# Kernel optimization log

Hardware: AMD Instinct MI355X
Metric: run time of the kernel (lower is better)

## Reference

```python
import jax, jax.numpy as jnp
import numpy as np

HEAD_DIM = 64
SCALE = 1.0 / np.sqrt(HEAD_DIM).astype(np.float32)


def setup_inputs() -> dict:
    key = jax.random.key(0)
    kq, kk, kv = jax.random.split(key, 3)
    shape = (2, 16, 2048, HEAD_DIM)  # [batch, num_heads, seq_len, head_dim]
    q = jax.random.normal(kq, shape, dtype=jnp.float32)
    k = jax.random.normal(kk, shape, dtype=jnp.float32)
    v = jax.random.normal(kv, shape, dtype=jnp.float32)
    # causal mask: True above the diagonal means 'masked' (no attention)
    mask = jnp.triu(jnp.ones((2048, 2048), dtype=bool), k=1)
    return {"q": q, "k": k, "v": v, "mask": mask}


def reference(q, k, v, mask):
    # scores: [b, h, s, s]
    scores = jnp.einsum("bhqd,bhkd->bhqk", q, k) * SCALE
    scores = jnp.where(mask[None, None, :, :], -jnp.inf, scores)
    attn_weights = jax.nn.softmax(scores, axis=-1)
    attn_weights = jnp.where(mask[None, None, :, :], 0.0, attn_weights)
    output = jnp.einsum("bhqk,bhkd->bhqd", attn_weights, v)
    return (output, attn_weights)
```

## Files before the change

### kernel.cpp

```cpp
#include <hip/hip_runtime.h>
#include <stdint.h>


#define SEQ 2048
#define HD  64
#define NBH 32

typedef __attribute__((ext_vector_type(8))) short short8;
typedef __attribute__((ext_vector_type(4))) float f32x4;

static __device__ __forceinline__ short f2bf(float x) {
  uint32_t u = __builtin_bit_cast(uint32_t, x);
  u = (u + 0x7FFFu + ((u >> 16) & 1u)) >> 16;
  return (short)(uint16_t)u;
}
static __device__ __forceinline__ float bf2f(short h) {
  uint32_t u = ((uint32_t)(uint16_t)h) << 16;
  return __builtin_bit_cast(float, u);
}
static __device__ __forceinline__ int swz(int row, int col) {
  return (row << 6) + (col ^ ((row & 7) << 3));
}

#define MFMA16(a, b, c) __builtin_amdgcn_mfma_f32_16x16x32_bf16((a), (b), (c), 0, 0, 0)

#define GLOAD16(gsrc, ldst)                                             \
  __builtin_amdgcn_global_load_lds(                                     \
      (const __attribute__((address_space(1))) void*)(gsrc),            \
      (__attribute__((address_space(3))) void*)(ldst), 16, 0, 0)

static __device__ __forceinline__ void cvt4(const f32x4 x, short8& h, short8& l,
                                            const int base) {
#pragma unroll
  for (int j = 0; j < 4; ++j) {
    const float fv = x[j];
    const short hb = f2bf(fv);
    h[base + j] = hb;
    l[base + j] = f2bf(fv - bf2f(hb));
  }
}

__global__ void prep_k(const float* __restrict__ K, short* __restrict__ Kh,
                       short* __restrict__ Kl) {
  const int gidx = blockIdx.x * 256 + threadIdx.x;
  const int row = gidx >> 3, g = gidx & 7;
  const f32x4* s = (const f32x4*)(K + (size_t)row * HD + g * 8);
  short8 h, l;
  cvt4(s[0], h, l, 0);
  cvt4(s[1], h, l, 4);
  const size_t di = (size_t)row * HD + ((g ^ (row & 7)) << 3);
  *(short8*)&Kh[di] = h;
  *(short8*)&Kl[di] = l;
}

__global__ void prep_v(const float* __restrict__ V, short* __restrict__ Vh,
                       short* __restrict__ Vl) {
  __shared__ float t[64][65];
  const int bh = blockIdx.x >> 5, kt = blockIdx.x & 31;
  const float* src = V + ((size_t)bh * SEQ + kt * 64) * HD;
#pragma unroll
  for (int i = 0; i < 4; ++i) {
    const int ch = threadIdx.x + i * 256;
    const int r = ch >> 4, c4 = (ch & 15) << 2;
    const f32x4 x = *(const f32x4*)(src + r * HD + c4);
#pragma unroll
    for (int j = 0; j < 4; ++j) t[r][c4 + j] = x[j];
  }
  __syncthreads();
#pragma unroll
  for (int i = 0; i < 2; ++i) {
    const int oid = threadIdx.x + i * 256;
    const int d = oid >> 3, g = oid & 7;
    f32x4 a, b;
#pragma unroll
    for (int j = 0; j < 4; ++j) {
      a[j] = t[g * 8 + j][d];
      b[j] = t[g * 8 + 4 + j][d];
    }
    short8 h, l;
    cvt4(a, h, l, 0);
    cvt4(b, h, l, 4);
    const size_t di = ((size_t)bh * HD + d) * SEQ + kt * 64 + ((g ^ (d & 7)) << 3);
    *(short8*)&Vh[di] = h;
    *(short8*)&Vl[di] = l;
  }
}

__global__ __launch_bounds__(256, 2) void attn_fwd(
    const float* __restrict__ gq,
    const short* __restrict__ gKh, const short* __restrict__ gKl,
    const short* __restrict__ gVh, const short* __restrict__ gVl,
    float* __restrict__ go, float* __restrict__ ga) {
  __shared__ __align__(16) short lK[2][2][4096];
  __shared__ __align__(16) short lV[2][2][4096];
  __shared__ __align__(16) short lP[2][4][1024];

  const int tid  = threadIdx.x;
  const int w    = tid >> 6;
  const int lane = tid & 63;
  const int lg   = lane >> 4;
  const int ln   = lane & 15;

  const int bh = blockIdx.x >> 4;
  const int z  = blockIdx.x & 15;

  const float* qp  = gq  + (size_t)bh * SEQ * HD;
  const short* Khb = gKh + (size_t)bh * SEQ * HD;
  const short* Klb = gKl + (size_t)bh * SEQ * HD;
  const short* Vhb = gVh + (size_t)bh * SEQ * HD;
  const short* Vlb = gVl + (size_t)bh * SEQ * HD;
  float* op = go + (size_t)bh * SEQ * HD;
  float* ap = ga + (size_t)bh * SEQ * SEQ;

  auto stage_k = [&](const short* th, const short* tl, short* bh_, short* bl_) {
    const int o0 = w * 1024 + lane * 8;
    GLOAD16(th + o0,       bh_ + w * 1024);
    GLOAD16(th + o0 + 512, bh_ + w * 1024 + 512);
    GLOAD16(tl + o0,       bl_ + w * 1024);
    GLOAD16(tl + o0 + 512, bl_ + w * 1024 + 512);
  };
  auto stage_v = [&](const short* th, const short* tl, short* bh_, short* bl_) {
    const int c0 = w * 128 + lane;
    const int c1 = c0 + 64;
    GLOAD16(th + (size_t)(c0 >> 3) * SEQ + (c0 & 7) * 8, bh_ + w * 1024);
    GLOAD16(th + (size_t)(c1 >> 3) * SEQ + (c1 & 7) * 8, bh_ + w * 1024 + 512);
    GLOAD16(tl + (size_t)(c0 >> 3) * SEQ + (c0 & 7) * 8, bl_ + w * 1024);
    GLOAD16(tl + (size_t)(c1 >> 3) * SEQ + (c1 & 7) * 8, bl_ + w * 1024 + 512);
  };

  for (int sec = 0; sec < 2; ++sec) {
    const int qb     = (sec == 0) ? (31 - z) : z;
    const int qbase  = qb << 6;
    const int wqbase = qbase + (w << 4);

    short8 qh[2], ql[2];
    {
      const float* qrow = qp + (size_t)(wqbase + ln) * HD;
#pragma unroll
      for (int c = 0; c < 2; ++c) {
        const int d0 = c * 32 + lg * 8;
        const f32x4 x0 = *(const f32x4*)(qrow + d0);
        const f32x4 x1 = *(const f32x4*)(qrow + d0 + 4);
#pragma unroll
        for (int j = 0; j < 4; ++j) {
          float xs = x0[j] * 0.125f;
          short hb = f2bf(xs);
          qh[c][j] = hb;
          ql[c][j] = f2bf(xs - bf2f(hb));
          xs = x1[j] * 0.125f;
          hb = f2bf(xs);
          qh[c][4 + j] = hb;
          ql[c][4 + j] = f2bf(xs - bf2f(hb));
        }
      }
    }

    f32x4 oacc[4];
    const f32x4 Z4 = {0.f, 0.f, 0.f, 0.f};
#pragma unroll
    for (int n = 0; n < 4; ++n) oacc[n] = Z4;
    float lpart[4] = {0.f, 0.f, 0.f, 0.f};

    stage_k(Khb, Klb, lK[0][0], lK[0][1]);
    stage_v(Vhb, Vlb, lV[0][0], lV[0][1]);
    __syncthreads();
    int cur = 0;
    for (int kt = 0; kt <= qb; ++kt, cur ^= 1) {
      if (kt < qb) {
        stage_k(Khb + (kt + 1) * 4096, Klb + (kt + 1) * 4096,
                lK[cur ^ 1][0], lK[cur ^ 1][1]);
        stage_v(Vhb + (kt + 1) * 64, Vlb + (kt + 1) * 64,
                lV[cur ^ 1][0], lV[cur ^ 1][1]);
      }
      const short* bKh = lK[cur][0];
      const short* bKl = lK[cur][1];
      const short* bVh = lV[cur][0];
      const short* bVl = lV[cur][1];

      f32x4 sc[4];
#pragma unroll
      for (int n = 0; n < 4; ++n) {
        f32x4 acc = Z4;
#pragma unroll
        for (int c = 0; c < 2; ++c) {
          const int bi = swz(n * 16 + ln, c * 32 + lg * 8);
          const short8 kh = *(const short8*)&bKh[bi];
          const short8 kl = *(const short8*)&bKl[bi];
          acc = MFMA16(qh[c], kh, acc);
          acc = MFMA16(ql[c], kh, acc);
          acc = MFMA16(qh[c], kl, acc);
        }
        sc[n] = acc;
      }

#pragma unroll
      for (int n = 0; n < 4; ++n) {
        const int kg = (kt << 6) + n * 16 + ln;
#pragma unroll
        for (int r = 0; r < 4; ++r) {
          const int qg = wqbase + lg * 4 + r;
          const float e = (kg <= qg) ? __expf(sc[n][r]) : 0.f;
          lpart[r] += e;
          const short eh = f2bf(e);
          const short el = f2bf(e - bf2f(eh));
          const int pi = swz(lg * 4 + r, n * 16 + ln);
          lP[0][w][pi] = eh;
          lP[1][w][pi] = el;
        }
      }
      asm volatile("s_waitcnt lgkmcnt(0)" ::: "memory");
      __builtin_amdgcn_sched_barrier(0);

#pragma unroll
      for (int c = 0; c < 2; ++c) {
        const int ac = swz(ln, c * 32 + lg * 8);
        const short8 ph = *(const short8*)&lP[0][w][ac];
        const short8 pl = *(const short8*)&lP[1][w][ac];
#pragma unroll
        for (int n = 0; n < 4; ++n) {
          const int bi = swz(n * 16 + ln, c * 32 + lg * 8);
          const short8 vh = *(const short8*)&bVh[bi];
          const short8 vl = *(const short8*)&bVl[bi];
          oacc[n] = MFMA16(ph, vh, oacc[n]);
          oacc[n] = MFMA16(pl, vh, oacc[n]);
          oacc[n] = MFMA16(ph, vl, oacc[n]);
        }
      }
      __syncthreads();
    }

    float linv[4];
#pragma unroll
    for (int r = 0; r < 4; ++r) {
      float s = lpart[r];
      s += __shfl_xor(s, 8, 64);
      s += __shfl_xor(s, 4, 64);
      s += __shfl_xor(s, 2, 64);
      s += __shfl_xor(s, 1, 64);
      linv[r] = 1.0f / s;
    }

#pragma unroll
    for (int n = 0; n < 4; ++n)
#pragma unroll
      for (int r = 0; r < 4; ++r)
        __builtin_nontemporal_store(oacc[n][r] * linv[r],
            &op[(size_t)(wqbase + lg * 4 + r) * HD + n * 16 + ln]);

    stage_k(Khb, Klb, lK[0][0], lK[0][1]);
    __syncthreads();
    cur = 0;
    for (int kt = 0; kt <= qb; ++kt, cur ^= 1) {
      if (kt < qb)
        stage_k(Khb + (kt + 1) * 4096, Klb + (kt + 1) * 4096,
                lK[cur ^ 1][0], lK[cur ^ 1][1]);
      const short* bKh = lK[cur][0];
      const short* bKl = lK[cur][1];

      f32x4 sc[4];
#pragma unroll
      for (int n = 0; n < 4; ++n) {
        f32x4 acc = Z4;
#pragma unroll
        for (int c = 0; c < 2; ++c) {
          const int bi = swz(n * 16 + ln, c * 32 + lg * 8);
          const short8 kh = *(const short8*)&bKh[bi];
          const short8 kl = *(const short8*)&bKl[bi];
          acc = MFMA16(qh[c], kh, acc);
          acc = MFMA16(ql[c], kh, acc);
          acc = MFMA16(qh[c], kl, acc);
        }
        sc[n] = acc;
      }

#pragma unroll
      for (int n = 0; n < 4; ++n) {
        const int kg = (kt << 6) + n * 16 + ln;
#pragma unroll
        for (int r = 0; r < 4; ++r) {
          const int qg = wqbase + lg * 4 + r;
          const float pv = (kg <= qg) ? __expf(sc[n][r]) * linv[r] : 0.f;
          __builtin_nontemporal_store(pv, &ap[(size_t)qg * SEQ + kg]);
        }
      }
      __syncthreads();
    }

    const int zstart = (qb + 1) << 6;
    const int zc = SEQ - zstart;
    if (zc > 0) {
      for (int row = 0; row < 64; ++row) {
        float* dst = ap + (size_t)(qbase + row) * SEQ + zstart;
        for (int c = tid * 4; c < zc; c += 1024) {
          float* p = dst + c;
          __builtin_nontemporal_store(0.0f, p + 0);
          __builtin_nontemporal_store(0.0f, p + 1);
          __builtin_nontemporal_store(0.0f, p + 2);
          __builtin_nontemporal_store(0.0f, p + 3);
        }
      }
    }
  }
}

extern "C" void kernel_launch(void* const* d_in, const int* in_sizes, int n_in,
                              void* d_out, int out_size, void* d_ws, size_t ws_size,
                              hipStream_t stream) {
  (void)in_sizes; (void)n_in; (void)out_size; (void)ws_size;
  const float* q = (const float*)d_in[0];
  const float* k = (const float*)d_in[1];
  const float* v = (const float*)d_in[2];
  float* o = (float*)d_out;
  float* a = o + (size_t)NBH * SEQ * HD;

  short* Khi  = (short*)d_ws;
  short* Klo  = Khi  + (size_t)NBH * SEQ * HD;
  short* Vthi = Klo  + (size_t)NBH * SEQ * HD;
  short* Vtlo = Vthi + (size_t)NBH * SEQ * HD;

  prep_k<<<dim3(2048), dim3(256), 0, stream>>>(k, Khi, Klo);
  prep_v<<<dim3(1024), dim3(256), 0, stream>>>(v, Vthi, Vtlo);
  attn_fwd<<<dim3(512), dim3(256), 0, stream>>>(q, Khi, Klo, Vthi, Vtlo, o, a);
}
```

Before: 704.3 us.

## Restructure attention into 128-thread blocks with 32-key tiles and per-wave 32 query rows

Each block now has 2 waves handling one 64-row query tile, with each wave owning 32 query rows. Key tiles shrink to 32, and the grid grows to 1024 blocks, replacing the paired-section scheme with a direct mapping from block to query tile. The P tile is kept in LDS as fp32 and split into bf16 hi/lo on read, and the LDS swizzle moves from the prep kernels into the staging addresses. Zero-fill of the masked region uses vector stores. This is meant to raise MFMA reuse per loaded K/V fragment and improve occupancy and load balance, at the cost of more barriers per key and register pressure from doubled accumulators.

```diff
diff --git a/kernel.cpp b/kernel.cpp
--- a/kernel.cpp
+++ b/kernel.cpp
@@ -17,9 +17,6 @@
 static __device__ __forceinline__ float bf2f(short h) {
   uint32_t u = ((uint32_t)(uint16_t)h) << 16;
   return __builtin_bit_cast(float, u);
-}
-static __device__ __forceinline__ int swz(int row, int col) {
-  return (row << 6) + (col ^ ((row & 7) << 3));
 }
 
 #define MFMA16(a, b, c) __builtin_amdgcn_mfma_f32_16x16x32_bf16((a), (b), (c), 0, 0, 0)
@@ -48,7 +45,7 @@
   short8 h, l;
   cvt4(s[0], h, l, 0);
   cvt4(s[1], h, l, 4);
-  const size_t di = (size_t)row * HD + ((g ^ (row & 7)) << 3);
+  const size_t di = (size_t)row * HD + g * 8;
   *(short8*)&Kh[di] = h;
   *(short8*)&Kl[di] = l;
 }
@@ -80,20 +77,20 @@
     short8 h, l;
     cvt4(a, h, l, 0);
     cvt4(b, h, l, 4);
-    const size_t di = ((size_t)bh * HD + d) * SEQ + kt * 64 + ((g ^ (d & 7)) << 3);
+    const size_t di = ((size_t)bh * HD + d) * SEQ + kt * 64 + g * 8;
     *(short8*)&Vh[di] = h;
     *(short8*)&Vl[di] = l;
   }
 }
 
-__global__ __launch_bounds__(256, 2) void attn_fwd(
+__global__ __launch_bounds__(128, 2) void attn_fwd(
     const float* __restrict__ gq,
     const short* __restrict__ gKh, const short* __restrict__ gKl,
     const short* __restrict__ gVh, const short* __restrict__ gVl,
     float* __restrict__ go, float* __restrict__ ga) {
-  __shared__ __align__(16) short lK[2][2][4096];
-  __shared__ __align__(16) short lV[2][2][4096];
-  __shared__ __align__(16) short lP[2][4][1024];
+  __shared__ __align__(16) short lK[2][2][2048];
+  __shared__ __align__(16) short lVt[2][2][2048];
+  __shared__ __align__(16) float lP[2][1024];
 
   const int tid  = threadIdx.x;
   const int w    = tid >> 6;
@@ -101,8 +98,10 @@
   const int lg   = lane >> 4;
   const int ln   = lane & 15;
 
-  const int bh = blockIdx.x >> 4;
-  const int z  = blockIdx.x & 15;
+  const int i  = blockIdx.x >> 5;
+  const int bh = blockIdx.x & 31;
+  const int s  = (i < 16) ? (31 - i) : (i - 16);
+  const int nt = 2 * s + 2;
 
   const float* qp  = gq  + (size_t)bh * SEQ * HD;
   const short* Khb = gKh + (size_t)bh * SEQ * HD;
@@ -112,193 +111,215 @@
   float* op = go + (size_t)bh * SEQ * HD;
   float* ap = ga + (size_t)bh * SEQ * SEQ;
 
-  auto stage_k = [&](const short* th, const short* tl, short* bh_, short* bl_) {
-    const int o0 = w * 1024 + lane * 8;
-    GLOAD16(th + o0,       bh_ + w * 1024);
-    GLOAD16(th + o0 + 512, bh_ + w * 1024 + 512);
-    GLOAD16(tl + o0,       bl_ + w * 1024);
-    GLOAD16(tl + o0 + 512, bl_ + w * 1024 + 512);
+  const int wqb = s * 64 + w * 32;
+
+  short8 qh[2][2], ql[2][2];
+#pragma unroll
+  for (int gq2 = 0; gq2 < 2; ++gq2) {
+    const float* qrow = qp + (size_t)(wqb + gq2 * 16 + ln) * HD;
+#pragma unroll
+    for (int c = 0; c < 2; ++c) {
+      const int d0 = c * 32 + lg * 8;
+      const f32x4 x0 = *(const f32x4*)(qrow + d0);
+      const f32x4 x1 = *(const f32x4*)(qrow + d0 + 4);
+#pragma unroll
+      for (int j = 0; j < 4; ++j) {
+        float xs = x0[j] * 0.125f;
+        short hb = f2bf(xs);
+        qh[gq2][c][j] = hb;
+        ql[gq2][c][j] = f2bf(xs - bf2f(hb));
+        xs = x1[j] * 0.125f;
+        hb = f2bf(xs);
+        qh[gq2][c][4 + j] = hb;
+        ql[gq2][c][4 + j] = f2bf(xs - bf2f(hb));
+      }
+    }
+  }
+
+  auto stage_k = [&](int kt, int buf) {
+#pragma unroll
+    for (int j2 = 0; j2 < 2; ++j2) {
+      const int kr   = w * 16 + j2 * 8 + (lane >> 3);
+      const int sblk = (lane & 7) ^ (kr & 7);
+      const size_t so = (size_t)(kt * 32 + kr) * HD + sblk * 8;
+      GLOAD16(Khb + so, &lK[buf][0][w * 1024 + j2 * 512]);
+      GLOAD16(Klb + so, &lK[buf][1][w * 1024 + j2 * 512]);
+    }
   };
-  auto stage_v = [&](const short* th, const short* tl, short* bh_, short* bl_) {
-    const int c0 = w * 128 + lane;
-    const int c1 = c0 + 64;
-    GLOAD16(th + (size_t)(c0 >> 3) * SEQ + (c0 & 7) * 8, bh_ + w * 1024);
-    GLOAD16(th + (size_t)(c1 >> 3) * SEQ + (c1 & 7) * 8, bh_ + w * 1024 + 512);
-    GLOAD16(tl + (size_t)(c0 >> 3) * SEQ + (c0 & 7) * 8, bl_ + w * 1024);
-    GLOAD16(tl + (size_t)(c1 >> 3) * SEQ + (c1 & 7) * 8, bl_ + w * 1024 + 512);
+  auto stage_v = [&](int kt, int buf) {
+#pragma unroll
+    for (int j2 = 0; j2 < 2; ++j2) {
+      const int d   = j2 * 32 + w * 16 + (lane >> 2);
+      const int skb = (lane & 3) ^ ((d >> 1) & 3);
+      const size_t so = (size_t)d * SEQ + kt * 32 + skb * 8;
+      GLOAD16(Vhb + so, &lVt[buf][0][j2 * 1024 + w * 512]);
+      GLOAD16(Vlb + so, &lVt[buf][1][j2 * 1024 + w * 512]);
+    }
   };
 
-  for (int sec = 0; sec < 2; ++sec) {
-    const int qb     = (sec == 0) ? (31 - z) : z;
-    const int qbase  = qb << 6;
-    const int wqbase = qbase + (w << 4);
-
-    short8 qh[2], ql[2];
-    {
-      const float* qrow = qp + (size_t)(wqbase + ln) * HD;
+  f32x4 oacc[2][4];
+  const f32x4 Z4 = {0.f, 0.f, 0.f, 0.f};
+#pragma unroll
+  for (int a = 0; a < 2; ++a)
+#pragma unroll
+    for (int n = 0; n < 4; ++n) oacc[a][n] = Z4;
+  float lpart[2][4] = {{0.f, 0.f, 0.f, 0.f}, {0.f, 0.f, 0.f, 0.f}};
+
+  stage_k(0, 0);
+  stage_v(0, 0);
+  __syncthreads();
+  for (int kt = 0; kt < nt; ++kt) {
+    const int cur = kt & 1;
+    if (kt + 1 < nt) {
+      stage_k(kt + 1, cur ^ 1);
+      stage_v(kt + 1, cur ^ 1);
+    }
+
+    short8 kh[2][2], kl[2][2];
+#pragma unroll
+    for (int n = 0; n < 2; ++n)
 #pragma unroll
       for (int c = 0; c < 2; ++c) {
-        const int d0 = c * 32 + lg * 8;
-        const f32x4 x0 = *(const f32x4*)(qrow + d0);
-        const f32x4 x1 = *(const f32x4*)(qrow + d0 + 4);
-#pragma unroll
-        for (int j = 0; j < 4; ++j) {
-          float xs = x0[j] * 0.125f;
-          short hb = f2bf(xs);
-          qh[c][j] = hb;
-          ql[c][j] = f2bf(xs - bf2f(hb));
-          xs = x1[j] * 0.125f;
-          hb = f2bf(xs);
-          qh[c][4 + j] = hb;
-          ql[c][4 + j] = f2bf(xs - bf2f(hb));
+        const int off = (n * 16 + ln) * HD + (((c * 4 + lg) ^ (ln & 7)) * 8);
+        kh[n][c] = *(const short8*)&lK[cur][0][off];
+        kl[n][c] = *(const short8*)&lK[cur][1][off];
+      }
+    f32x4 sc[2][2];
+#pragma unroll
+    for (int g2 = 0; g2 < 2; ++g2)
+#pragma unroll
+      for (int n = 0; n < 2; ++n) {
+        f32x4 acc = Z4;
+#pragma unroll
+        for (int c = 0; c < 2; ++c) {
+          acc = MFMA16(qh[g2][c], kh[n][c], acc);
+          acc = MFMA16(ql[g2][c], kh[n][c], acc);
+          acc = MFMA16(qh[g2][c], kl[n][c], acc);
         }
-      }
-    }
-
-    f32x4 oacc[4];
-    const f32x4 Z4 = {0.f, 0.f, 0.f, 0.f};
-#pragma unroll
-    for (int n = 0; n < 4; ++n) oacc[n] = Z4;
-    float lpart[4] = {0.f, 0.f, 0.f, 0.f};
-
-    stage_k(Khb, Klb, lK[0][0], lK[0][1]);
-    stage_v(Vhb, Vlb, lV[0][0], lV[0][1]);
+        sc[g2][n] = acc;
+      }
+
+#pragma unroll
+    for (int g2 = 0; g2 < 2; ++g2)
+#pragma unroll
+      for (int n = 0; n < 2; ++n) {
+        const int kg = kt * 32 + n * 16 + ln;
+#pragma unroll
+        for (int r = 0; r < 4; ++r) {
+          const int qg = wqb + g2 * 16 + lg * 4 + r;
+          const float e = (kg <= qg) ? __expf(sc[g2][n][r]) : 0.f;
+          lpart[g2][r] += e;
+          const int row = g2 * 16 + lg * 4 + r;
+          const int col = (n * 16 + ln) ^ ((row & 7) << 2);
+          lP[w][row * 32 + col] = e;
+        }
+      }
+    asm volatile("s_waitcnt lgkmcnt(0)" ::: "memory");
+    __builtin_amdgcn_sched_barrier(0);
+
+    short8 ph[2], pl[2];
+#pragma unroll
+    for (int g2 = 0; g2 < 2; ++g2) {
+      const int row = g2 * 16 + ln;
+      const int m   = (ln & 7) << 2;
+      const float* base = &lP[w][row * 32];
+      const f32x4 a0 = *(const f32x4*)&base[(lg * 8) ^ m];
+      const f32x4 a1 = *(const f32x4*)&base[((lg * 8) ^ m) ^ 4];
+#pragma unroll
+      for (int j = 0; j < 4; ++j) {
+        short hb = f2bf(a0[j]);
+        ph[g2][j] = hb;
+        pl[g2][j] = f2bf(a0[j] - bf2f(hb));
+        hb = f2bf(a1[j]);
+        ph[g2][4 + j] = hb;
+        pl[g2][4 + j] = f2bf(a1[j] - bf2f(hb));
+      }
+    }
+    short8 vh[4], vl[4];
+#pragma unroll
+    for (int nd = 0; nd < 4; ++nd) {
+      const int d   = nd * 16 + ln;
+      const int off = d * 32 + ((lg ^ ((d >> 1) & 3)) * 8);
+      vh[nd] = *(const short8*)&lVt[cur][0][off];
+      vl[nd] = *(const short8*)&lVt[cur][1][off];
+    }
+#pragma unroll
+    for (int g2 = 0; g2 < 2; ++g2)
+#pragma unroll
+      for (int nd = 0; nd < 4; ++nd) {
+        oacc[g2][nd] = MFMA16(ph[g2], vh[nd], oacc[g2][nd]);
+        oacc[g2][nd] = MFMA16(pl[g2], vh[nd], oacc[g2][nd]);
+        oacc[g2][nd] = MFMA16(ph[g2], vl[nd], oacc[g2][nd]);
+      }
     __syncthreads();
-    int cur = 0;
-    for (int kt = 0; kt <= qb; ++kt, cur ^= 1) {
-      if (kt < qb) {
-        stage_k(Khb + (kt + 1) * 4096, Klb + (kt + 1) * 4096,
-                lK[cur ^ 1][0], lK[cur ^ 1][1]);
-        stage_v(Vhb + (kt + 1) * 64, Vlb + (kt + 1) * 64,
-                lV[cur ^ 1][0], lV[cur ^ 1][1]);
-      }
-      const short* bKh = lK[cur][0];
-      const short* bKl = lK[cur][1];
-      const short* bVh = lV[cur][0];
-      const short* bVl = lV[cur][1];
-
-      f32x4 sc[4];
-#pragma unroll
-      for (int n = 0; n < 4; ++n) {
+  }
+
+  float linv[2][4];
+#pragma unroll
+  for (int g2 = 0; g2 < 2; ++g2)
+#pragma unroll
+    for (int r = 0; r < 4; ++r) {
+      float sm = lpart[g2][r];
+      sm += __shfl_xor(sm, 8, 64);
+      sm += __shfl_xor(sm, 4, 64);
+      sm += __shfl_xor(sm, 2, 64);
+      sm += __shfl_xor(sm, 1, 64);
+      linv[g2][r] = 1.0f / sm;
+    }
+
+#pragma unroll
+  for (int g2 = 0; g2 < 2; ++g2)
+#pragma unroll
+    for (int nd = 0; nd < 4; ++nd)
+#pragma unroll
+      for (int r = 0; r < 4; ++r)
+        __builtin_nontemporal_store(oacc[g2][nd][r] * linv[g2][r],
+            &op[(size_t)(wqb + g2 * 16 + lg * 4 + r) * HD + nd * 16 + ln]);
+
+  stage_k(0, 0);
+  __syncthreads();
+  for (int kt = 0; kt < nt; ++kt) {
+    const int cur = kt & 1;
+    if (kt + 1 < nt) stage_k(kt + 1, cur ^ 1);
+
+    short8 kh[2][2], kl[2][2];
+#pragma unroll
+    for (int n = 0; n < 2; ++n)
+#pragma unroll
+      for (int c = 0; c < 2; ++c) {
+        const int off = (n * 16 + ln) * HD + (((c * 4 + lg) ^ (ln & 7)) * 8);
+        kh[n][c] = *(const short8*)&lK[cur][0][off];
+        kl[n][c] = *(const short8*)&lK[cur][1][off];
+      }
+#pragma unroll
+    for (int g2 = 0; g2 < 2; ++g2)
+#pragma unroll
+      for (int n = 0; n < 2; ++n) {
         f32x4 acc = Z4;
 #pragma unroll
         for (int c = 0; c < 2; ++c) {
-          const int bi = swz(n * 16 + ln, c * 32 + lg * 8);
-          const short8 kh = *(const short8*)&bKh[bi];
-          const short8 kl = *(const short8*)&bKl[bi];
-          acc = MFMA16(qh[c], kh, acc);
-          acc = MFMA16(ql[c], kh, acc);
-          acc = MFMA16(qh[c], kl, acc);
+          acc = MFMA16(qh[g2][c], kh[n][c], acc);
+          acc = MFMA16(ql[g2][c], kh[n][c], acc);
+          acc = MFMA16(qh[g2][c], kl[n][c], acc);
         }
-        sc[n] = acc;
-      }
-
-#pragma unroll
-      for (int n = 0; n < 4; ++n) {
-        const int kg = (kt << 6) + n * 16 + ln;
+        const int kg = kt * 32 + n * 16 + ln;
 #pragma unroll
         for (int r = 0; r < 4; ++r) {
-          const int qg = wqbase + lg * 4 + r;
-          const float e = (kg <= qg) ? __expf(sc[n][r]) : 0.f;
-          lpart[r] += e;
-          const short eh = f2bf(e);
-          const short el = f2bf(e - bf2f(eh));
-          const int pi = swz(lg * 4 + r, n * 16 + ln);
-          lP[0][w][pi] = eh;
-          lP[1][w][pi] = el;
-        }
-      }
-      asm volatile("s_waitcnt lgkmcnt(0)" ::: "memory");
-      __builtin_amdgcn_sched_barrier(0);
-
-#pragma unroll
-      for (int c = 0; c < 2; ++c) {
-        const int ac = swz(ln, c * 32 + lg * 8);
-        const short8 ph = *(const short8*)&lP[0][w][ac];
-        const short8 pl = *(const short8*)&lP[1][w][ac];
-#pragma unroll
-        for (int n = 0; n < 4; ++n) {
-          const int bi = swz(n * 16 + ln, c * 32 + lg * 8);
-          const short8 vh = *(const short8*)&bVh[bi];
-          const short8 vl = *(const short8*)&bVl[bi];
-          oacc[n] = MFMA16(ph, vh, oacc[n]);
-          oacc[n] = MFMA16(pl, vh, oacc[n]);
-          oacc[n] = MFMA16(ph, vl, oacc[n]);
-        }
-      }
-      __syncthreads();
-    }
-
-    float linv[4];
-#pragma unroll
-    for (int r = 0; r < 4; ++r) {
-      float s = lpart[r];
-      s += __shfl_xor(s, 8, 64);
-      s += __shfl_xor(s, 4, 64);
-      s += __shfl_xor(s, 2, 64);
-      s += __shfl_xor(s, 1, 64);
-      linv[r] = 1.0f / s;
-    }
-
-#pragma unroll
-    for (int n = 0; n < 4; ++n)
-#pragma unroll
-      for (int r = 0; r < 4; ++r)
-        __builtin_nontemporal_store(oacc[n][r] * linv[r],
-            &op[(size_t)(wqbase + lg * 4 + r) * HD + n * 16 + ln]);
-
-    stage_k(Khb, Klb, lK[0][0], lK[0][1]);
-    __syncthreads();
-    cur = 0;
-    for (int kt = 0; kt <= qb; ++kt, cur ^= 1) {
-      if (kt < qb)
-        stage_k(Khb + (kt + 1) * 4096, Klb + (kt + 1) * 4096,
-                lK[cur ^ 1][0], lK[cur ^ 1][1]);
-      const short* bKh = lK[cur][0];
-      const short* bKl = lK[cur][1];
-
-      f32x4 sc[4];
-#pragma unroll
-      for (int n = 0; n < 4; ++n) {
-        f32x4 acc = Z4;
-#pragma unroll
-        for (int c = 0; c < 2; ++c) {
-          const int bi = swz(n * 16 + ln, c * 32 + lg * 8);
-          const short8 kh = *(const short8*)&bKh[bi];
-          const short8 kl = *(const short8*)&bKl[bi];
-          acc = MFMA16(qh[c], kh, acc);
-          acc = MFMA16(ql[c], kh, acc);
-          acc = MFMA16(qh[c], kl, acc);
-        }
-        sc[n] = acc;
-      }
-
-#pragma unroll
-      for (int n = 0; n < 4; ++n) {
-        const int kg = (kt << 6) + n * 16 + ln;
-#pragma unroll
-        for (int r = 0; r < 4; ++r) {
-          const int qg = wqbase + lg * 4 + r;
-          const float pv = (kg <= qg) ? __expf(sc[n][r]) * linv[r] : 0.f;
+          const int qg = wqb + g2 * 16 + lg * 4 + r;
+          const float pv = (kg <= qg) ? __expf(acc[r]) * linv[g2][r] : 0.f;
           __builtin_nontemporal_store(pv, &ap[(size_t)qg * SEQ + kg]);
         }
       }
-      __syncthreads();
-    }
-
-    const int zstart = (qb + 1) << 6;
-    const int zc = SEQ - zstart;
-    if (zc > 0) {
-      for (int row = 0; row < 64; ++row) {
-        float* dst = ap + (size_t)(qbase + row) * SEQ + zstart;
-        for (int c = tid * 4; c < zc; c += 1024) {
-          float* p = dst + c;
-          __builtin_nontemporal_store(0.0f, p + 0);
-          __builtin_nontemporal_store(0.0f, p + 1);
-          __builtin_nontemporal_store(0.0f, p + 2);
-          __builtin_nontemporal_store(0.0f, p + 3);
-        }
-      }
+    __syncthreads();
+  }
+
+  const int zstart = nt * 32;
+  const int zc = SEQ - zstart;
+  if (zc > 0) {
+    for (int row = 0; row < 64; ++row) {
+      float* dst = ap + (size_t)(s * 64 + row) * SEQ + zstart;
+      for (int c = tid * 4; c < zc; c += 512)
+        __builtin_nontemporal_store(Z4, (f32x4*)(dst + c));
     }
   }
 }
@@ -320,5 +341,5 @@
 
   prep_k<<<dim3(2048), dim3(256), 0, stream>>>(k, Khi, Klo);
   prep_v<<<dim3(1024), dim3(256), 0, stream>>>(v, Vthi, Vtlo);
-  attn_fwd<<<dim3(512), dim3(256), 0, stream>>>(q, Khi, Klo, Vthi, Vtlo, o, a);
-}
+  attn_fwd<<<dim3(1024), dim3(128), 0, stream>>>(q, Khi, Klo, Vthi, Vtlo, o, a);
+}
```

Measured after the change: 703.4 us. No clear change (-0.1%).
